# Optimization experiments

Hardware: AMD Instinct MI355X
Metric: run time of the kernel (lower is better)

The kernel has to match this reference:

```python
import jax, jax.numpy as jnp
import numpy as np

S, B, D = 2048, 2, 1024
H, HD = 16, 64  # head_num, head_dim
SCALE = 1.0 / (HD ** 0.5)


def setup_inputs() -> dict:
    key = jax.random.key(0)
    ks = jax.random.split(key, 7)
    std = 1.0 / np.sqrt(D)
    return {
        "inputs": jax.random.normal(ks[0], (S, B, D), dtype=jnp.float32),
        "Wkv": jax.random.uniform(ks[1], (D, 2 * H * HD), jnp.float32, -std, std),
        "bkv": jax.random.uniform(ks[2], (2 * H * HD,), jnp.float32, -std, std),
        "Wq": jax.random.uniform(ks[3], (D, H * HD), jnp.float32, -std, std),
        "bq": jax.random.uniform(ks[4], (H * HD,), jnp.float32, -std, std),
        "Wp": jax.random.uniform(ks[5], (H * HD, D), jnp.float32, -std, std),
        "bp": jax.random.uniform(ks[6], (D,), jnp.float32, -std, std),
    }


def reference(inputs, Wkv, bkv, Wq, bq, Wp, bp):
    s, b, _ = inputs.shape
    kv = inputs @ Wkv + bkv                      # [S,B,2*H*HD]
    k, v = jnp.split(kv, 2, axis=-1)
    q = inputs @ Wq + bq                         # [S,B,H*HD]
    k = k.reshape(s, b, H, HD)
    q = q.reshape(s, b, H, HD)
    v = v.reshape(s, b, H, HD)
    # scores: [B,H,S,S]
    attn = jnp.einsum("sbhd,tbhd->bhst", q, k) * SCALE
    attn = jax.nn.softmax(attn, axis=-1)         # dropout is identity in eval
    attn_vec = jnp.einsum("bhst,tbhd->sbhd", attn, v)
    attn_vec = attn_vec.reshape(s, b, H * HD)
    return attn_vec @ Wp + bp                    # [S,B,D]
```

## Files before the change

### kernel.cpp

```cpp
#include <hip/hip_runtime.h>
#include <hip/hip_bf16.h>
#include <stdint.h>


typedef __bf16 bf16_t;
typedef __bf16 bf16x8 __attribute__((ext_vector_type(8)));
typedef __bf16 bf16x4 __attribute__((ext_vector_type(4)));
typedef __bf16 bf16x2 __attribute__((ext_vector_type(2)));
typedef float f32x4 __attribute__((ext_vector_type(4)));
typedef float f32x16 __attribute__((ext_vector_type(16)));
typedef uint32_t u32;

#define S_LEN 2048
#define BATCH 2
#define DMODEL 1024
#define NHEAD 16
#define HDIM 64
#define KVB 64
#define FNT (S_LEN / KVB)
#define Q_SCALE 0.1803368801111204f

__device__ inline void gld16(const void* g, void* l)
{
    __builtin_amdgcn_global_load_lds(
        (const __attribute__((address_space(1))) void*)g,
        (__attribute__((address_space(3))) void*)l, 16, 0, 0);
}

__device__ inline u32 pack2(float a, float b)
{
    union { bf16x2 h; u32 u; } c;
    c.h[0] = (bf16_t)a; c.h[1] = (bf16_t)b;
    return c.u;
}

__global__ __launch_bounds__(256) void xcvt_kernel(
    const float* __restrict__ in, bf16_t* __restrict__ out)
{
    size_t i = ((size_t)blockIdx.x * 256 + threadIdx.x) * 8;
    float4 f0 = *(const float4*)(in + i);
    float4 f1 = *(const float4*)(in + i + 4);
    bf16x8 o;
    o[0] = (bf16_t)f0.x; o[1] = (bf16_t)f0.y; o[2] = (bf16_t)f0.z; o[3] = (bf16_t)f0.w;
    o[4] = (bf16_t)f1.x; o[5] = (bf16_t)f1.y; o[6] = (bf16_t)f1.z; o[7] = (bf16_t)f1.w;
    *(bf16x8*)(out + i) = o;
}

__global__ __launch_bounds__(256) void transpose_convert(
    const float* __restrict__ in, bf16_t* __restrict__ out, int K, int N)
{
    __shared__ float tile[64][65];
    int n0 = blockIdx.x * 64, k0 = blockIdx.y * 64;
    int r = threadIdx.x >> 2;
    int c = (threadIdx.x & 3) * 16;
    const float* src = in + (size_t)(k0 + r) * N + n0 + c;
#pragma unroll
    for (int j = 0; j < 16; j += 4) {
        float4 f = *(const float4*)(src + j);
        tile[r][c + j + 0] = f.x;
        tile[r][c + j + 1] = f.y;
        tile[r][c + j + 2] = f.z;
        tile[r][c + j + 3] = f.w;
    }
    __syncthreads();
    bf16x8 o0, o1;
#pragma unroll
    for (int j = 0; j < 8; ++j) o0[j] = (bf16_t)tile[c + j][r];
#pragma unroll
    for (int j = 0; j < 8; ++j) o1[j] = (bf16_t)tile[c + 8 + j][r];
    bf16_t* dst = out + (size_t)(n0 + r) * K + k0 + c;
    *(bf16x8*)dst = o0;
    *(bf16x8*)(dst + 8) = o1;
}

__global__ __launch_bounds__(256) void gemm_qkv(
    const bf16_t* __restrict__ A, const bf16_t* __restrict__ WT,
    const float* __restrict__ bkv, const float* __restrict__ bq,
    bf16_t* __restrict__ outK, bf16_t* __restrict__ outV,
    bf16_t* __restrict__ outQ)
{
    const int K = 1024;
    __shared__ bf16_t As[128 * 32];
    __shared__ bf16_t Bs[128 * 32];
    int tid = threadIdx.x;
    int wave = tid >> 6, lane = tid & 63;
    int l15 = lane & 15, l4 = lane >> 4;
    int m0 = blockIdx.x * 128, n0 = blockIdx.y * 128;
    int wr = (wave >> 1) * 64, wc = (wave & 1) * 64;

    bf16_t* ldsT = (wave < 2) ? As : Bs;
    const bf16_t* gbase = (wave < 2) ? A : WT;
    int rbase = (wave & 1) * 64;
    int tile0 = (wave < 2) ? m0 : n0;
    int srow = lane >> 2;
    int scol = (lane & 3) * 8;

    f32x4 acc[4][4] = {};

    for (int k0 = 0; k0 < K; k0 += 32) {
#pragma unroll
        for (int j = 0; j < 4; ++j) {
            const bf16_t* g = gbase +
                (size_t)(tile0 + rbase + j * 16 + srow) * K + k0 + scol;
            gld16(g, ldsT + (rbase + j * 16) * 32);
        }
        __syncthreads();
        bf16x8 af[4], bfr[4];
#pragma unroll
        for (int i = 0; i < 4; ++i)
            af[i] = *(const bf16x8*)&As[(wr + i * 16 + l15) * 32 + l4 * 8];
#pragma unroll
        for (int i = 0; i < 4; ++i)
            bfr[i] = *(const bf16x8*)&Bs[(wc + i * 16 + l15) * 32 + l4 * 8];
#pragma unroll
        for (int mi = 0; mi < 4; ++mi)
#pragma unroll
            for (int ni = 0; ni < 4; ++ni)
                acc[mi][ni] = __builtin_amdgcn_mfma_f32_16x16x32_bf16(
                    af[mi], bfr[ni], acc[mi][ni], 0, 0, 0);
        __syncthreads();
    }

#pragma unroll
    for (int mi = 0; mi < 4; ++mi) {
#pragma unroll
        for (int ni = 0; ni < 4; ++ni) {
#pragma unroll
            for (int e = 0; e < 4; ++e) {
                int gm = m0 + wr + mi * 16 + l4 * 4 + e;
                int gn = n0 + wc + ni * 16 + l15;
                float bsel = (gn < 2048) ? bkv[gn] : bq[gn - 2048];
                float v = acc[mi][ni][e] + bsel;
                int s = gm >> 1, b = gm & 1;
                int nn = gn & 1023;
                int h = nn >> 6, d = nn & 63;
                size_t idx = ((size_t)((b << 4) + h) * S_LEN + s) * HDIM + d;
                if (gn < 1024)
                    outK[idx] = (bf16_t)v;
                else if (gn < 2048)
                    outV[idx] = (bf16_t)v;
                else
                    outQ[idx] = (bf16_t)(v * Q_SCALE);
            }
        }
    }
}

__global__ __launch_bounds__(256) void gemm_out_kernel(
    const bf16_t* __restrict__ A, const bf16_t* __restrict__ WT,
    const float* __restrict__ bias, float* __restrict__ outF)
{
    const int K = 1024, N = 1024;
    __shared__ bf16_t As[64 * 32];
    __shared__ bf16_t Bs[128 * 32];
    int tid = threadIdx.x, wave = tid >> 6, lane = tid & 63;
    int l15 = lane & 15, l4 = lane >> 4;
    int m0 = blockIdx.x * 64, n0 = blockIdx.y * 128;
    int wc = wave * 32;
    int srow = lane >> 2, scol = (lane & 3) * 8;

    f32x4 acc[4][2] = {};

    for (int k0 = 0; k0 < K; k0 += 32) {
#pragma unroll
        for (int j = 0; j < 3; ++j) {
            int slot = wave * 3 + j;
            const bf16_t* g;
            bf16_t* l;
            if (slot < 4) {
                g = A + (size_t)(m0 + slot * 16 + srow) * K + k0 + scol;
                l = As + slot * 512;
            } else {
                g = WT + (size_t)(n0 + (slot - 4) * 16 + srow) * K + k0 + scol;
                l = Bs + (slot - 4) * 512;
            }
            gld16(g, l);
        }
        __syncthreads();
        bf16x8 af[4], bfr[2];
#pragma unroll
        for (int i = 0; i < 4; ++i)
            af[i] = *(const bf16x8*)&As[(i * 16 + l15) * 32 + l4 * 8];
#pragma unroll
        for (int i = 0; i < 2; ++i)
            bfr[i] = *(const bf16x8*)&Bs[(wc + i * 16 + l15) * 32 + l4 * 8];
#pragma unroll
        for (int mi = 0; mi < 4; ++mi)
#pragma unroll
            for (int ni = 0; ni < 2; ++ni)
                acc[mi][ni] = __builtin_amdgcn_mfma_f32_16x16x32_bf16(
                    af[mi], bfr[ni], acc[mi][ni], 0, 0, 0);
        __syncthreads();
    }

#pragma unroll
    for (int mi = 0; mi < 4; ++mi)
#pragma unroll
        for (int ni = 0; ni < 2; ++ni)
#pragma unroll
            for (int e = 0; e < 4; ++e) {
                int gm = m0 + mi * 16 + l4 * 4 + e;
                int gn = n0 + wc + ni * 16 + l15;
                outF[(size_t)gm * N + gn] = acc[mi][ni][e] + bias[gn];
            }
}

__global__ __launch_bounds__(256) void flash_kernel(
    const bf16_t* __restrict__ Qb, const bf16_t* __restrict__ Kb,
    const bf16_t* __restrict__ Vb, bf16_t* __restrict__ AVb)
{
    __shared__ __align__(16) char lds[34816];
    char* KsB = lds;
    bf16_t* VtB = (bf16_t*)(lds + 16384);

    int bh = blockIdx.y;
    int tid = threadIdx.x, wave = tid >> 6, lane = tid & 63;
    int l31 = lane & 31, hi = lane >> 5;

    const bf16_t* Qp = Qb + (size_t)bh * S_LEN * HDIM;
    const bf16_t* Kp = Kb + (size_t)bh * S_LEN * HDIM;
    const bf16_t* Vp = Vb + (size_t)bh * S_LEN * HDIM;

    int q0 = blockIdx.x * 128 + wave * 32;

    bf16x8 qf[4];
#pragma unroll
    for (int dc = 0; dc < 4; ++dc)
        qf[dc] = *(const bf16x8*)(Qp + (size_t)(q0 + l31) * HDIM + dc * 16 + hi * 8);

    f32x16 acc0 = {}, acc1 = {};
    float l_run = 0.f;

    int krow = lane >> 3;
    int kcb = ((lane & 7) << 4) ^ (krow << 4);
    int vd = (tid >> 4) * 4;
    int vt = (tid & 15) * 2;
    bf16x4 vreg[2][2];
    int swz = (l31 & 7) << 4;

#define STAGE_K(it, buf)                                                       \
    {                                                                          \
        _Pragma("unroll")                                                      \
        for (int j = 0; j < 2; ++j) {                                          \
            int t = wave * 16 + j * 8 + krow;                                  \
            const char* g = (const char*)Kp +                                  \
                ((size_t)((it) * KVB + t) * HDIM) * 2 + kcb;                   \
            gld16(g, KsB + (buf) * 8192 + (wave * 16 + j * 8) * 128);          \
        }                                                                      \
    }
#define LOAD_V(it)                                                             \
    {                                                                          \
        const bf16_t* vb = Vp + (size_t)((it) * KVB + vt) * HDIM + vd;         \
        vreg[0][0] = *(const bf16x4*)vb;                                       \
        vreg[0][1] = *(const bf16x4*)(vb + HDIM);                              \
        vreg[1][0] = *(const bf16x4*)(vb + 32 * HDIM);                         \
        vreg[1][1] = *(const bf16x4*)(vb + 33 * HDIM);                         \
    }
#define WRITE_V(buf)                                                           \
    {                                                                          \
        bf16_t* vtb = VtB + (buf) * 4608;                                      \
        _Pragma("unroll")                                                      \
        for (int p = 0; p < 2; ++p) {                                          \
            _Pragma("unroll")                                                  \
            for (int j = 0; j < 4; ++j) {                                      \
                bf16x2 w;                                                      \
                w[0] = vreg[p][0][j];                                          \
                w[1] = vreg[p][1][j];                                          \
                *(bf16x2*)&vtb[(vd + j) * 72 + vt + 32 * p] = w;               \
            }                                                                  \
        }                                                                      \
    }

    STAGE_K(0, 0);
    LOAD_V(0);
    WRITE_V(0);
    __syncthreads();

    for (int it = 0; it < FNT; ++it) {
        int cur = it & 1;
        if (it + 1 < FNT) {
            STAGE_K(it + 1, cur ^ 1);
            LOAD_V(it + 1);
        }

        f32x16 s0 = {}, s1 = {};
        __builtin_amdgcn_s_setprio(1);
#pragma unroll
        for (int dc = 0; dc < 4; ++dc) {
            bf16x8 k0 = *(const bf16x8*)(KsB + cur * 8192 + l31 * 128 +
                                         ((dc * 32 + hi * 16) ^ swz));
            bf16x8 k1 = *(const bf16x8*)(KsB + cur * 8192 + (32 + l31) * 128 +
                                         ((dc * 32 + hi * 16) ^ swz));
            s0 = __builtin_amdgcn_mfma_f32_32x32x16_bf16(k0, qf[dc], s0, 0, 0, 0);
            s1 = __builtin_amdgcn_mfma_f32_32x32x16_bf16(k1, qf[dc], s1, 0, 0, 0);
        }
        __builtin_amdgcn_s_setprio(0);

#pragma unroll
        for (int r = 0; r < 16; ++r) s0[r] = __builtin_amdgcn_exp2f(s0[r]);
#pragma unroll
        for (int r = 0; r < 16; ++r) s1[r] = __builtin_amdgcn_exp2f(s1[r]);
        float a8[8];
#pragma unroll
        for (int r = 0; r < 8; ++r)
            a8[r] = (s0[r] + s0[r + 8]) + (s1[r] + s1[r + 8]);
        float rs = ((a8[0] + a8[1]) + (a8[2] + a8[3])) +
                   ((a8[4] + a8[5]) + (a8[6] + a8[7]));
        rs += __shfl_xor(rs, 32);
        l_run += rs;

        __builtin_amdgcn_s_setprio(1);
#pragma unroll
        for (int s = 0; s < 4; ++s) {
            const int base = 8 * (s & 1);
            f32x16& P = (s < 2) ? s0 : s1;
            u32 a0 = pack2(P[base + 0], P[base + 1]);
            u32 a1 = pack2(P[base + 2], P[base + 3]);
            u32 b0 = pack2(P[base + 4], P[base + 5]);
            u32 b1 = pack2(P[base + 6], P[base + 7]);
            asm("v_permlane32_swap_b32 %0, %1" : "+v"(a0), "+v"(b0));
            asm("v_permlane32_swap_b32 %0, %1" : "+v"(a1), "+v"(b1));
            union { u32 u[4]; bf16x8 v; } pa;
            pa.u[0] = a0; pa.u[1] = a1; pa.u[2] = b0; pa.u[3] = b1;
            const bf16_t* vtb = VtB + cur * 4608;
            bf16x8 va0 = *(const bf16x8*)&vtb[l31 * 72 + s * 16 + hi * 8];
            bf16x8 va1 = *(const bf16x8*)&vtb[(32 + l31) * 72 + s * 16 + hi * 8];
            acc0 = __builtin_amdgcn_mfma_f32_32x32x16_bf16(va0, pa.v, acc0, 0, 0, 0);
            acc1 = __builtin_amdgcn_mfma_f32_32x32x16_bf16(va1, pa.v, acc1, 0, 0, 0);
        }
        __builtin_amdgcn_s_setprio(0);

        if (it + 1 < FNT) WRITE_V(cur ^ 1);
        __syncthreads();
    }

    bf16_t* sw = (bf16_t*)lds + wave * (32 * 72);
    float inv = 1.0f / l_run;
#pragma unroll
    for (int g = 0; g < 4; ++g) {
        bf16x4 w0, w1;
#pragma unroll
        for (int e = 0; e < 4; ++e) {
            w0[e] = (bf16_t)(acc0[4 * g + e] * inv);
            w1[e] = (bf16_t)(acc1[4 * g + e] * inv);
        }
        int d0 = 8 * g + 4 * hi;
        *(bf16x4*)&sw[l31 * 72 + d0] = w0;
        *(bf16x4*)&sw[l31 * 72 + 32 + d0] = w1;
    }
    __syncthreads();
    {
        int q = lane >> 1, half = lane & 1;
        const bf16_t* srow = sw + q * 72 + half * 32;
        int s = q0 + q;
        int b = bh >> 4, h = bh & 15;
        bf16_t* dst = AVb + ((size_t)s * BATCH + b) * DMODEL + h * HDIM + half * 32;
#pragma unroll
        for (int k = 0; k < 4; ++k)
            *(bf16x8*)(dst + k * 8) = *(const bf16x8*)(srow + k * 8);
    }
}

extern "C" void kernel_launch(void* const* d_in, const int* in_sizes, int n_in,
                              void* d_out, int out_size, void* d_ws, size_t ws_size,
                              hipStream_t stream)
{
    const float* X   = (const float*)d_in[0];
    const float* Wkv = (const float*)d_in[1];
    const float* bkv = (const float*)d_in[2];
    const float* Wq  = (const float*)d_in[3];
    const float* bq  = (const float*)d_in[4];
    const float* Wp  = (const float*)d_in[5];
    const float* bp  = (const float*)d_in[6];
    float* out = (float*)d_out;

    char* ws = (char*)d_ws;
    size_t off = 0;
    auto alloc = [&](size_t bytes) -> void* {
        void* p = ws + off;
        off += (bytes + 255) & ~(size_t)255;
        return p;
    };
    bf16_t* WqkvT = (bf16_t*)alloc((size_t)3072 * 1024 * 2);
    bf16_t* WpT   = (bf16_t*)alloc((size_t)1024 * 1024 * 2);
    bf16_t* Qb    = (bf16_t*)alloc((size_t)32 * S_LEN * HDIM * 2);
    bf16_t* Kb    = (bf16_t*)alloc((size_t)32 * S_LEN * HDIM * 2);
    bf16_t* Vb    = (bf16_t*)alloc((size_t)32 * S_LEN * HDIM * 2);
    bf16_t* Xbf   = (bf16_t*)alloc((size_t)4096 * 1024 * 2);
    bf16_t* AVb   = (bf16_t*)alloc((size_t)4096 * 1024 * 2);

    xcvt_kernel<<<2048, 256, 0, stream>>>(X, Xbf);
    transpose_convert<<<dim3(32, 16), 256, 0, stream>>>(Wkv, WqkvT, 1024, 2048);
    transpose_convert<<<dim3(16, 16), 256, 0, stream>>>(
        Wq, WqkvT + (size_t)2048 * 1024, 1024, 1024);
    transpose_convert<<<dim3(16, 16), 256, 0, stream>>>(Wp, WpT, 1024, 1024);

    gemm_qkv<<<dim3(32, 24), 256, 0, stream>>>(Xbf, WqkvT, bkv, bq, Kb, Vb, Qb);
    flash_kernel<<<dim3(S_LEN / 128, 32), 256, 0, stream>>>(Qb, Kb, Vb, AVb);
    gemm_out_kernel<<<dim3(64, 8), 256, 0, stream>>>(AVb, WpT, bp, out);
}
```

Baseline: 134.2 us.

## Split flash KV loop across two wave groups and remap blocks for XCD locality

The flash kernel now runs 512 threads per block. Two groups of four waves each handle half of the KV sequence for the same queries, and their partial accumulators and row sums are merged through LDS at the end. This doubles the parallelism per query tile and halves the serial KV loop length. In exchange it uses twice the LDS and adds an extra reduction step. Both GEMMs and the flash kernel also launch as 1D grids with a block-id swizzle (bid&7), which groups neighbouring tiles on the same XCD for L2 reuse. The merge is valid only because the softmax apparently uses no running max, so partial sums can be added directly.

```diff
diff --git a/kernel.cpp b/kernel.cpp
--- a/kernel.cpp
+++ b/kernel.cpp
@@ -17,7 +17,7 @@
 #define NHEAD 16
 #define HDIM 64
 #define KVB 64
-#define FNT (S_LEN / KVB)
+#define HITER 16
 #define Q_SCALE 0.1803368801111204f
 
 __device__ inline void gld16(const void* g, void* l)
@@ -85,7 +85,9 @@
     int tid = threadIdx.x;
     int wave = tid >> 6, lane = tid & 63;
     int l15 = lane & 15, l4 = lane >> 4;
-    int m0 = blockIdx.x * 128, n0 = blockIdx.y * 128;
+    int bid = blockIdx.x;
+    int id = (bid & 7) * 96 + (bid >> 3);
+    int m0 = (id / 24) * 128, n0 = (id % 24) * 128;
     int wr = (wave >> 1) * 64, wc = (wave & 1) * 64;
 
     bf16_t* ldsT = (wave < 2) ? As : Bs;
@@ -155,7 +157,9 @@
     __shared__ bf16_t Bs[128 * 32];
     int tid = threadIdx.x, wave = tid >> 6, lane = tid & 63;
     int l15 = lane & 15, l4 = lane >> 4;
-    int m0 = blockIdx.x * 64, n0 = blockIdx.y * 128;
+    int bid = blockIdx.x;
+    int id = (bid & 7) * 64 + (bid >> 3);
+    int m0 = (id >> 3) * 64, n0 = (id & 7) * 128;
     int wc = wave * 32;
     int srow = lane >> 2, scol = (lane & 3) * 8;
 
@@ -205,23 +209,33 @@
             }
 }
 
-__global__ __launch_bounds__(256) void flash_kernel(
+__global__ __launch_bounds__(512) void flash_kernel(
     const bf16_t* __restrict__ Qb, const bf16_t* __restrict__ Kb,
     const bf16_t* __restrict__ Vb, bf16_t* __restrict__ AVb)
 {
-    __shared__ __align__(16) char lds[34816];
-    char* KsB = lds;
-    bf16_t* VtB = (bf16_t*)(lds + 16384);
-
-    int bh = blockIdx.y;
+    __shared__ __align__(16) char lds[69632];
+
+    int bid = blockIdx.x;
+    int id = (bid & 7) * 64 + (bid >> 3);
+    int bh = id >> 4;
+    int qx = id & 15;
+
     int tid = threadIdx.x, wave = tid >> 6, lane = tid & 63;
+    int group = wave >> 2;
+    int wg = wave & 3;
+    int tg = tid & 255;
     int l31 = lane & 31, hi = lane >> 5;
 
+    char* KsB = lds + group * 34816;
+    bf16_t* VtB = (bf16_t*)(KsB + 16384);
+
     const bf16_t* Qp = Qb + (size_t)bh * S_LEN * HDIM;
-    const bf16_t* Kp = Kb + (size_t)bh * S_LEN * HDIM;
-    const bf16_t* Vp = Vb + (size_t)bh * S_LEN * HDIM;
-
-    int q0 = blockIdx.x * 128 + wave * 32;
+    const bf16_t* Kp = Kb + (size_t)bh * S_LEN * HDIM
+                          + (size_t)group * HITER * KVB * HDIM;
+    const bf16_t* Vp = Vb + (size_t)bh * S_LEN * HDIM
+                          + (size_t)group * HITER * KVB * HDIM;
+
+    int q0 = qx * 128 + wg * 32;
 
     bf16x8 qf[4];
 #pragma unroll
@@ -233,8 +247,8 @@
 
     int krow = lane >> 3;
     int kcb = ((lane & 7) << 4) ^ (krow << 4);
-    int vd = (tid >> 4) * 4;
-    int vt = (tid & 15) * 2;
+    int vd = (tg >> 4) * 4;
+    int vt = (tg & 15) * 2;
     bf16x4 vreg[2][2];
     int swz = (l31 & 7) << 4;
 
@@ -242,10 +256,10 @@
     {                                                                          \
         _Pragma("unroll")                                                      \
         for (int j = 0; j < 2; ++j) {                                          \
-            int t = wave * 16 + j * 8 + krow;                                  \
+            int t = wg * 16 + j * 8 + krow;                                    \
             const char* g = (const char*)Kp +                                  \
                 ((size_t)((it) * KVB + t) * HDIM) * 2 + kcb;                   \
-            gld16(g, KsB + (buf) * 8192 + (wave * 16 + j * 8) * 128);          \
+            gld16(g, KsB + (buf) * 8192 + (wg * 16 + j * 8) * 128);            \
         }                                                                      \
     }
 #define LOAD_V(it)                                                             \
@@ -276,9 +290,9 @@
     WRITE_V(0);
     __syncthreads();
 
-    for (int it = 0; it < FNT; ++it) {
+    for (int it = 0; it < HITER; ++it) {
         int cur = it & 1;
-        if (it + 1 < FNT) {
+        if (it + 1 < HITER) {
             STAGE_K(it + 1, cur ^ 1);
             LOAD_V(it + 1);
         }
@@ -330,26 +344,47 @@
         }
         __builtin_amdgcn_s_setprio(0);
 
-        if (it + 1 < FNT) WRITE_V(cur ^ 1);
+        if (it + 1 < HITER) WRITE_V(cur ^ 1);
         __syncthreads();
     }
 
-    bf16_t* sw = (bf16_t*)lds + wave * (32 * 72);
-    float inv = 1.0f / l_run;
-#pragma unroll
-    for (int g = 0; g < 4; ++g) {
-        bf16x4 w0, w1;
-#pragma unroll
-        for (int e = 0; e < 4; ++e) {
-            w0[e] = (bf16_t)(acc0[4 * g + e] * inv);
-            w1[e] = (bf16_t)(acc1[4 * g + e] * inv);
-        }
-        int d0 = 8 * g + 4 * hi;
-        *(bf16x4*)&sw[l31 * 72 + d0] = w0;
-        *(bf16x4*)&sw[l31 * 72 + 32 + d0] = w1;
+    float* xch = (float*)lds;
+    float* lxch = (float*)(lds + 32768);
+    if (group == 1) {
+        float* base = xch + wg * 2048;
+#pragma unroll
+        for (int r = 0; r < 16; ++r) base[r * 64 + lane] = acc0[r];
+#pragma unroll
+        for (int r = 0; r < 16; ++r) base[(16 + r) * 64 + lane] = acc1[r];
+        lxch[wg * 64 + lane] = l_run;
     }
     __syncthreads();
-    {
+    if (group == 0) {
+        float* base = xch + wg * 2048;
+#pragma unroll
+        for (int r = 0; r < 16; ++r) acc0[r] += base[r * 64 + lane];
+#pragma unroll
+        for (int r = 0; r < 16; ++r) acc1[r] += base[(16 + r) * 64 + lane];
+        l_run += lxch[wg * 64 + lane];
+
+        bf16_t* sw = (bf16_t*)(lds + 34816) + wg * (32 * 72);
+        float inv = 1.0f / l_run;
+#pragma unroll
+        for (int g = 0; g < 4; ++g) {
+            bf16x4 w0, w1;
+#pragma unroll
+            for (int e = 0; e < 4; ++e) {
+                w0[e] = (bf16_t)(acc0[4 * g + e] * inv);
+                w1[e] = (bf16_t)(acc1[4 * g + e] * inv);
+            }
+            int d0 = 8 * g + 4 * hi;
+            *(bf16x4*)&sw[l31 * 72 + d0] = w0;
+            *(bf16x4*)&sw[l31 * 72 + 32 + d0] = w1;
+        }
+    }
+    __syncthreads();
+    if (group == 0) {
+        bf16_t* sw = (bf16_t*)(lds + 34816) + wg * (32 * 72);
         int q = lane >> 1, half = lane & 1;
         const bf16_t* srow = sw + q * 72 + half * 32;
         int s = q0 + q;
@@ -395,7 +430,7 @@
         Wq, WqkvT + (size_t)2048 * 1024, 1024, 1024);
     transpose_convert<<<dim3(16, 16), 256, 0, stream>>>(Wp, WpT, 1024, 1024);
 
-    gemm_qkv<<<dim3(32, 24), 256, 0, stream>>>(Xbf, WqkvT, bkv, bq, Kb, Vb, Qb);
-    flash_kernel<<<dim3(S_LEN / 128, 32), 256, 0, stream>>>(Qb, Kb, Vb, AVb);
-    gemm_out_kernel<<<dim3(64, 8), 256, 0, stream>>>(AVb, WpT, bp, out);
-}
+    gemm_qkv<<<768, 256, 0, stream>>>(Xbf, WqkvT, bkv, bq, Kb, Vb, Qb);
+    flash_kernel<<<512, 512, 0, stream>>>(Qb, Kb, Vb, AVb);
+    gemm_out_kernel<<<512, 256, 0, stream>>>(AVb, WpT, bp, out);
+}
```

Measured after the change: 139.8 us. 4.2% more time.

## Double GEMM K-step to 64 and XOR-swizzle LDS tiles in projection GEMMs

Applied to the files above, without the earlier changes.

Both the QKV and output projection GEMMs now stage 64-wide K slices per iteration instead of 32, which halves the number of barrier pairs per tile. LDS rows become 128 bytes with an XOR swizzle on the 16-byte chunk index, applied on the global-to-LDS load side and undone on the fragment reads, to avoid bank conflicts. LDS use per block doubles, which may reduce occupancy. The staging stays single-buffered.

```diff
diff --git a/kernel.cpp b/kernel.cpp
--- a/kernel.cpp
+++ b/kernel.cpp
@@ -80,44 +80,49 @@
     bf16_t* __restrict__ outQ)
 {
     const int K = 1024;
-    __shared__ bf16_t As[128 * 32];
-    __shared__ bf16_t Bs[128 * 32];
+    __shared__ __align__(16) char AsB[128 * 128];
+    __shared__ __align__(16) char BsB[128 * 128];
     int tid = threadIdx.x;
     int wave = tid >> 6, lane = tid & 63;
     int l15 = lane & 15, l4 = lane >> 4;
     int m0 = blockIdx.x * 128, n0 = blockIdx.y * 128;
     int wr = (wave >> 1) * 64, wc = (wave & 1) * 64;
 
-    bf16_t* ldsT = (wave < 2) ? As : Bs;
+    char* ldsT = (wave < 2) ? AsB : BsB;
     const bf16_t* gbase = (wave < 2) ? A : WT;
     int rbase = (wave & 1) * 64;
     int tile0 = (wave < 2) ? m0 : n0;
-    int srow = lane >> 2;
-    int scol = (lane & 3) * 8;
+    int srow = lane >> 3;
+    int kcb = ((lane & 7) << 4) ^ (srow << 4);
+    int rx = (l15 & 7) << 4;
 
     f32x4 acc[4][4] = {};
 
-    for (int k0 = 0; k0 < K; k0 += 32) {
-#pragma unroll
-        for (int j = 0; j < 4; ++j) {
-            const bf16_t* g = gbase +
-                (size_t)(tile0 + rbase + j * 16 + srow) * K + k0 + scol;
-            gld16(g, ldsT + (rbase + j * 16) * 32);
+    for (int k0 = 0; k0 < K; k0 += 64) {
+#pragma unroll
+        for (int j = 0; j < 8; ++j) {
+            const char* g = (const char*)(gbase +
+                (size_t)(tile0 + rbase + j * 8 + srow) * K + k0) + kcb;
+            gld16(g, ldsT + (rbase + j * 8) * 128);
         }
         __syncthreads();
-        bf16x8 af[4], bfr[4];
-#pragma unroll
-        for (int i = 0; i < 4; ++i)
-            af[i] = *(const bf16x8*)&As[(wr + i * 16 + l15) * 32 + l4 * 8];
-#pragma unroll
-        for (int i = 0; i < 4; ++i)
-            bfr[i] = *(const bf16x8*)&Bs[(wc + i * 16 + l15) * 32 + l4 * 8];
-#pragma unroll
-        for (int mi = 0; mi < 4; ++mi)
-#pragma unroll
-            for (int ni = 0; ni < 4; ++ni)
-                acc[mi][ni] = __builtin_amdgcn_mfma_f32_16x16x32_bf16(
-                    af[mi], bfr[ni], acc[mi][ni], 0, 0, 0);
+#pragma unroll
+        for (int kk = 0; kk < 2; ++kk) {
+            int cb = (kk * 64 + l4 * 16) ^ rx;
+            bf16x8 af[4], bfr[4];
+#pragma unroll
+            for (int i = 0; i < 4; ++i)
+                af[i] = *(const bf16x8*)(AsB + (wr + i * 16 + l15) * 128 + cb);
+#pragma unroll
+            for (int i = 0; i < 4; ++i)
+                bfr[i] = *(const bf16x8*)(BsB + (wc + i * 16 + l15) * 128 + cb);
+#pragma unroll
+            for (int mi = 0; mi < 4; ++mi)
+#pragma unroll
+                for (int ni = 0; ni < 4; ++ni)
+                    acc[mi][ni] = __builtin_amdgcn_mfma_f32_16x16x32_bf16(
+                        af[mi], bfr[ni], acc[mi][ni], 0, 0, 0);
+        }
         __syncthreads();
     }
 
@@ -151,45 +156,51 @@
     const float* __restrict__ bias, float* __restrict__ outF)
 {
     const int K = 1024, N = 1024;
-    __shared__ bf16_t As[64 * 32];
-    __shared__ bf16_t Bs[128 * 32];
+    __shared__ __align__(16) char AsB[64 * 128];
+    __shared__ __align__(16) char BsB[128 * 128];
     int tid = threadIdx.x, wave = tid >> 6, lane = tid & 63;
     int l15 = lane & 15, l4 = lane >> 4;
     int m0 = blockIdx.x * 64, n0 = blockIdx.y * 128;
     int wc = wave * 32;
-    int srow = lane >> 2, scol = (lane & 3) * 8;
+    int srow = lane >> 3;
+    int kcb = ((lane & 7) << 4) ^ (srow << 4);
+    int rx = (l15 & 7) << 4;
 
     f32x4 acc[4][2] = {};
 
-    for (int k0 = 0; k0 < K; k0 += 32) {
-#pragma unroll
-        for (int j = 0; j < 3; ++j) {
-            int slot = wave * 3 + j;
+    for (int k0 = 0; k0 < K; k0 += 64) {
+#pragma unroll
+        for (int j = 0; j < 6; ++j) {
+            int slot = wave * 6 + j;
             const bf16_t* g;
-            bf16_t* l;
-            if (slot < 4) {
-                g = A + (size_t)(m0 + slot * 16 + srow) * K + k0 + scol;
-                l = As + slot * 512;
+            char* l;
+            if (slot < 8) {
+                g = A + (size_t)(m0 + slot * 8 + srow) * K + k0;
+                l = AsB + slot * 1024;
             } else {
-                g = WT + (size_t)(n0 + (slot - 4) * 16 + srow) * K + k0 + scol;
-                l = Bs + (slot - 4) * 512;
+                g = WT + (size_t)(n0 + (slot - 8) * 8 + srow) * K + k0;
+                l = BsB + (slot - 8) * 1024;
             }
-            gld16(g, l);
+            gld16((const char*)g + kcb, l);
         }
         __syncthreads();
-        bf16x8 af[4], bfr[2];
-#pragma unroll
-        for (int i = 0; i < 4; ++i)
-            af[i] = *(const bf16x8*)&As[(i * 16 + l15) * 32 + l4 * 8];
-#pragma unroll
-        for (int i = 0; i < 2; ++i)
-            bfr[i] = *(const bf16x8*)&Bs[(wc + i * 16 + l15) * 32 + l4 * 8];
-#pragma unroll
-        for (int mi = 0; mi < 4; ++mi)
-#pragma unroll
-            for (int ni = 0; ni < 2; ++ni)
-                acc[mi][ni] = __builtin_amdgcn_mfma_f32_16x16x32_bf16(
-                    af[mi], bfr[ni], acc[mi][ni], 0, 0, 0);
+#pragma unroll
+        for (int kk = 0; kk < 2; ++kk) {
+            int cb = (kk * 64 + l4 * 16) ^ rx;
+            bf16x8 af[4], bfr[2];
+#pragma unroll
+            for (int i = 0; i < 4; ++i)
+                af[i] = *(const bf16x8*)(AsB + (i * 16 + l15) * 128 + cb);
+#pragma unroll
+            for (int i = 0; i < 2; ++i)
+                bfr[i] = *(const bf16x8*)(BsB + (wc + i * 16 + l15) * 128 + cb);
+#pragma unroll
+            for (int mi = 0; mi < 4; ++mi)
+#pragma unroll
+                for (int ni = 0; ni < 2; ++ni)
+                    acc[mi][ni] = __builtin_amdgcn_mfma_f32_16x16x32_bf16(
+                        af[mi], bfr[ni], acc[mi][ni], 0, 0, 0);
+        }
         __syncthreads();
     }
 
```

Result: faster. 128.9 us (-4.0%).
